# Kernel optimization log

Measured on AMD Instinct MI355X. Metric: run time of the kernel, lower is better.

The kernel has to match this reference:

```python
import jax, jax.numpy as jnp
import numpy as np

EPS = 0.1           # entropic regularization epsilon
MAX_ITER = 100
THRESH = 0.1        # early-stop threshold on mean |u - u_prev|
LOG_EPS = 1e-8


def setup_inputs() -> dict:
    key = jax.random.key(0)
    kx, ky = jax.random.split(key)
    x = jax.random.normal(kx, (8, 1024, 3), dtype=jnp.float32)
    y = jax.random.normal(ky, (8, 1024, 3), dtype=jnp.float32)
    return {"x": x, "y": y}


def _sqdist(x, y):
    # squared euclidean cost matrix [B, N, N]  (== torch.cdist(x,y,p=2)**2)
    x2 = jnp.sum(x * x, axis=-1)[:, :, None]
    y2 = jnp.sum(y * y, axis=-1)[:, None, :]
    xy = jnp.einsum("bnd,bmd->bnm", x, y)
    return jnp.maximum(x2 + y2 - 2.0 * xy, 0.0)


def reference(x, y):
    B, N, D = x.shape
    C = _sqdist(x, y)                      # [B, N, N]
    log_mu = jnp.log(1.0 / N + LOG_EPS)    # scalar (uniform marginals)
    log_nu = log_mu

    u0 = jnp.zeros((B, N), dtype=x.dtype)
    v0 = jnp.zeros((B, N), dtype=x.dtype)

    def step(carry, _):
        u, v, done = carry
        # u-update uses old v
        M1 = (u[:, :, None] + v[:, None, :] - C) / EPS          # [B,N,N]
        u_new = EPS * (log_mu - jax.nn.logsumexp(M1, axis=-1)) + u
        # v-update uses new u
        M2 = (u_new[:, :, None] + v[:, None, :] - C) / EPS
        v_new = EPS * (log_nu - jax.nn.logsumexp(M2, axis=-2)) + v
        # freeze once converged (mimics torch early break)
        u_out = jnp.where(done, u, u_new)
        v_out = jnp.where(done, v, v_new)
        err = jnp.mean(jnp.abs(u_out - u))
        done_new = done | (err < THRESH)
        return (u_out, v_out, done_new), None

    (u, v, _), _ = jax.lax.scan(step, (u0, v0, jnp.array(False)), None, length=MAX_ITER)

    PI = jnp.exp((u[:, :, None] + v[:, None, :] - C) / EPS)     # transport plan
    emd = jnp.sum(PI * C, axis=(-2, -1))                        # [B]
    return jnp.mean(emd)                                        # reduction='mean'
```

## Files before the change

kernel.cpp:

```cpp
#include <hip/hip_runtime.h>

typedef unsigned int uint_t;

constexpr int B = 8;
constexpr int N = 1024;
constexpr int NBLOCKS = 256;
constexpr int NTHREADS = 1024;
constexpr int NWAVES = NTHREADS / 64;
constexpr int BPB = NBLOCKS / B;
constexpr int SEG = N / BPB;
constexpr int RPW = SEG / NWAVES;
constexpr int KPL = N / 64;
constexpr int MAX_ITER = 100;
constexpr float THRESH = 0.1f;
constexpr float K2 = 14.42695040888963f;
constexpr float A2K = 2.0f * K2;
constexpr float NEPSLN2 = -0.06931471805599453f;
constexpr float EPSLOGMU = -0.693146156565634f;
constexpr uint_t MAGIC = 0xC0FFEE01u;

constexpr int OFF_U      = 0;
constexpr int OFF_V      = OFF_U + B * N;
constexpr int OFF_ERRBLK = OFF_V + B * N;
constexpr int OFF_ERRBAT = OFF_ERRBLK + 256;
constexpr int OFF_EMDBLK = OFF_ERRBAT + 800;
constexpr int OFF_EMDBAT = OFF_EMDBLK + 256;
constexpr int OFF_ZERO   = OFF_EMDBAT + 8;
constexpr int OFF_BARFLG = OFF_ZERO;
constexpr int OFF_ERRFLG = OFF_BARFLG + 256;
constexpr int OFF_EMDFLG = OFF_ERRFLG + 8;
constexpr int OFF_ZEROEND= OFF_EMDFLG + 8;
constexpr int OFF_INIT   = OFF_ZEROEND;

__device__ __forceinline__ float gload(const float* p) {
  return __hip_atomic_load(p, __ATOMIC_RELAXED, __HIP_MEMORY_SCOPE_AGENT);
}
__device__ __forceinline__ void gstore(float* p, float v) {
  __hip_atomic_store(p, v, __ATOMIC_RELAXED, __HIP_MEMORY_SCOPE_AGENT);
}
__device__ __forceinline__ uint_t lflag(const uint_t* p) {
  return __hip_atomic_load(p, __ATOMIC_RELAXED, __HIP_MEMORY_SCOPE_AGENT);
}
__device__ __forceinline__ void sflag_rel(uint_t* p, uint_t v) {
  __hip_atomic_store(p, v, __ATOMIC_RELEASE, __HIP_MEMORY_SCOPE_AGENT);
}

__device__ __forceinline__ float wsum(float v) {
#pragma unroll
  for (int o = 32; o; o >>= 1) v += __shfl_xor(v, o);
  return v;
}
__device__ __forceinline__ float wmax(float v) {
#pragma unroll
  for (int o = 32; o; o >>= 1) v = fmaxf(v, __shfl_xor(v, o));
  return v;
}

__device__ __forceinline__ float block_sum(float v, float* sh) {
  v = wsum(v);
  const int wave = threadIdx.x >> 6;
  const int lane = threadIdx.x & 63;
  if (lane == 0) sh[wave] = v;
  __syncthreads();
  float tot = 0.f;
#pragma unroll
  for (int w = 0; w < NWAVES; ++w) tot += sh[w];
  __syncthreads();
  return tot;
}

__device__ __forceinline__ void batch_barrier(uint_t* flg, int seg, uint_t epoch,
                                              int lane) {
  __syncthreads();
  if (threadIdx.x == 0) sflag_rel(&flg[seg], epoch);
  if (threadIdx.x < 64) {
    for (;;) {
      uint_t f = (lane < BPB) ? lflag(&flg[lane]) : epoch;
      if (__all(f >= epoch)) break;
      __builtin_amdgcn_s_sleep(1);
    }
  }
  __syncthreads();
}

template <bool TRACK>
__device__ __forceinline__ float half_compute(
    const float* __restrict__ cx, const float* __restrict__ cy,
    const float* __restrict__ cz, const float* __restrict__ cw,
    const float* __restrict__ rx, const float* __restrict__ ry,
    const float* __restrict__ rz, const float* __restrict__ rw,
    const float* __restrict__ pin, const float* __restrict__ pout_old,
    float (&pnew)[RPW], int i0, int lane, bool pin_zero, bool first_out) {
  float p2[KPL];
#pragma unroll
  for (int k = 0; k < KPL; ++k)
    p2[k] = pin_zero ? 0.f : gload(&pin[lane + (k << 6)]) * K2;

  float a0[RPW], a1[RPW], a2[RPW], X[RPW], m[RPW];
  float vals[RPW][KPL];
#pragma unroll
  for (int rr = 0; rr < RPW; ++rr) {
    a0[rr] = A2K * rx[i0 + rr]; a1[rr] = A2K * ry[i0 + rr];
    a2[rr] = A2K * rz[i0 + rr];
    X[rr] = -rw[i0 + rr];
    m[rr] = -3.4e38f;
  }
#pragma unroll
  for (int k = 0; k < KPL; ++k) {
    const int j = lane + (k << 6);
    float ccx = cx[j], ccy = cy[j], ccz = cz[j];
    float base = cw[j] + p2[k];
#pragma unroll
    for (int rr = 0; rr < RPW; ++rr) {
      float t = fmaf(a0[rr], ccx, fmaf(a1[rr], ccy, fmaf(a2[rr], ccz, base)));
      float val = fminf(t - X[rr], p2[k]);
      vals[rr][k] = val;
      m[rr] = fmaxf(m[rr], val);
    }
  }
  float err = 0.f;
#pragma unroll
  for (int rr = 0; rr < RPW; ++rr) {
    float mr = wmax(m[rr]);
    float s = 0.f;
#pragma unroll
    for (int k = 0; k < KPL; ++k)
      s += __builtin_amdgcn_exp2f(vals[rr][k] - mr);
    s = wsum(s);
    float pn = fmaf(NEPSLN2, mr + __builtin_amdgcn_logf(s), EPSLOGMU);
    pnew[rr] = pn;
    if (TRACK && lane == 0) {
      float old = first_out ? 0.f : gload(&pout_old[i0 + rr]);
      err += fabsf(pn - old);
    }
  }
  return err;
}

__device__ __forceinline__ void store_rows(float* p, const float (&pnew)[RPW],
                                           int i0, int lane) {
  if (lane == 0) {
#pragma unroll
    for (int rr = 0; rr < RPW; ++rr) gstore(&p[i0 + rr], pnew[rr]);
  }
}

__global__ void __launch_bounds__(NTHREADS, 4) sinkhorn_kernel(
    const float* __restrict__ xg, const float* __restrict__ yg,
    float* __restrict__ out, float* __restrict__ ws) {
  __shared__ float s_xx[N], s_xy[N], s_xz[N], s_xw[N];
  __shared__ float s_yx[N], s_yy[N], s_yz[N], s_yw[N];
  __shared__ float sh_red[NWAVES];

  const int bid = blockIdx.x;
  const int tid = threadIdx.x;
  const int b = bid & 7;
  const int seg = bid >> 3;
  const int wave = tid >> 6;
  const int lane = tid & 63;
  const int i0 = seg * SEG + wave * RPW;

  float* u = ws + OFF_U + b * N;
  float* v = ws + OFF_V + b * N;
  float* err_blk = ws + OFF_ERRBLK + b * 32;
  float* err_bat = ws + OFF_ERRBAT;
  float* emd_blk = ws + OFF_EMDBLK + b * 32;
  float* emd_bat = ws + OFF_EMDBAT;
  uint_t* bar_flg = (uint_t*)(ws + OFF_BARFLG) + b * 32;
  uint_t* err_flg = (uint_t*)(ws + OFF_ERRFLG);
  uint_t* emd_flg = (uint_t*)(ws + OFF_EMDFLG);
  uint_t* init_flag = (uint_t*)(ws + OFF_INIT);

  if (bid == 0) {
    uint_t* zb = (uint_t*)(ws + OFF_ZERO);
    for (int i = tid; i < OFF_ZEROEND - OFF_ZERO; i += NTHREADS)
      __hip_atomic_store(&zb[i], 0u, __ATOMIC_RELAXED, __HIP_MEMORY_SCOPE_AGENT);
    __syncthreads();
    if (tid == 0) sflag_rel(init_flag, MAGIC);
  }

  for (int p = tid; p < N; p += NTHREADS) {
    const float* xp = xg + (size_t)(b * N + p) * 3;
    float x0 = xp[0], x1 = xp[1], x2 = xp[2];
    s_xx[p] = x0; s_xy[p] = x1; s_xz[p] = x2;
    s_xw[p] = -K2 * (x0 * x0 + x1 * x1 + x2 * x2);
    const float* yp = yg + (size_t)(b * N + p) * 3;
    float y0 = yp[0], y1 = yp[1], y2 = yp[2];
    s_yx[p] = y0; s_yy[p] = y1; s_yz[p] = y2;
    s_yw[p] = -K2 * (y0 * y0 + y1 * y1 + y2 * y2);
  }
  __syncthreads();

  float un[RPW];
  float my_err = half_compute<true>(s_yx, s_yy, s_yz, s_yw,
                                    s_xx, s_xy, s_xz, s_xw,
                                    v, u, un, i0, lane,
                                    true, true);
  store_rows(u, un, i0, lane);
  float blk_err = block_sum(my_err, sh_red);
  if (tid == 0) gstore(&err_blk[seg], blk_err);

  if (tid == 0 && bid != 0)
    while (lflag(init_flag) != MAGIC) __builtin_amdgcn_s_sleep(2);
  __syncthreads();

  uint_t epoch = 0;
  int it = 0;
  for (;;) {
    ++epoch;
    batch_barrier(bar_flg, seg, epoch, lane);

    float vn[RPW];
    half_compute<false>(s_xx, s_xy, s_xz, s_xw,
                        s_yx, s_yy, s_yz, s_yw,
                        u, nullptr, vn, i0, lane, false, false);
    store_rows(v, vn, i0, lane);

    if (seg == 0 && tid < 64) {
      float e = (lane < BPB) ? gload(&err_blk[lane]) : 0.f;
      e = wsum(e);
      if (lane == 0) {
        gstore(&err_bat[it * B + b], e);
        sflag_rel(&err_flg[b], (uint_t)(it + 1));
      }
    }
    ++epoch;
    batch_barrier(bar_flg, seg, epoch, lane);

    if (it == MAX_ITER - 1) break;

    my_err = half_compute<true>(s_yx, s_yy, s_yz, s_yw,
                                s_xx, s_xy, s_xz, s_xw,
                                v, u, un, i0, lane, false, false);

    if (tid < 64) {
      const uint_t want = (uint_t)(it + 1);
      for (;;) {
        uint_t f = (lane < B) ? lflag(&err_flg[lane]) : want;
        if (__all(f >= want)) break;
        __builtin_amdgcn_s_sleep(1);
      }
      float e = (lane < B) ? gload(&err_bat[it * B + lane]) : 0.f;
      e = wsum(e);
      if (lane == 0) sh_red[0] = e;
    }
    __syncthreads();
    float tot = sh_red[0];
    __syncthreads();
    if (tot * (1.f / (B * N)) < THRESH) break;

    store_rows(u, un, i0, lane);
    blk_err = block_sum(my_err, sh_red);
    if (tid == 0) gstore(&err_blk[seg], blk_err);
    ++it;
  }

  float p2e[KPL];
#pragma unroll
  for (int k = 0; k < KPL; ++k) p2e[k] = gload(&v[lane + (k << 6)]) * K2;
  float acc = 0.f;
#pragma unroll
  for (int rr = 0; rr < RPW; ++rr) {
    const int i = i0 + rr;
    float a0 = A2K * s_xx[i], a1 = A2K * s_xy[i], a2 = A2K * s_xz[i];
    float X = -s_xw[i];
    float u2 = gload(&u[i]) * K2;
#pragma unroll
    for (int k = 0; k < KPL; ++k) {
      const int j = lane + (k << 6);
      float t = fmaf(a0, s_yx[j], fmaf(a1, s_yy[j], fmaf(a2, s_yz[j], s_yw[j])));
      float kc = fmaxf(X - t, 0.f);
      acc = fmaf(__builtin_amdgcn_exp2f(u2 + p2e[k] - kc), kc, acc);
    }
  }
  float blk = block_sum(acc, sh_red);
  const uint_t ef = epoch + 1;
  if (tid == 0) { gstore(&emd_blk[seg], blk); sflag_rel(&bar_flg[seg], ef); }

  if (seg == 0 && tid < 64) {
    for (;;) {
      uint_t f = (lane < BPB) ? lflag(&bar_flg[lane]) : ef;
      if (__all(f >= ef)) break;
      __builtin_amdgcn_s_sleep(1);
    }
    float e = (lane < BPB) ? gload(&emd_blk[lane]) : 0.f;
    e = wsum(e);
    if (lane == 0) { gstore(&emd_bat[b], e); sflag_rel(&emd_flg[b], 1u); }
  }
  if (bid == 0 && tid < 64) {
    for (;;) {
      uint_t f = (lane < B) ? lflag(&emd_flg[lane]) : 1u;
      if (__all(f >= 1u)) break;
      __builtin_amdgcn_s_sleep(1);
    }
    float e = (lane < B) ? gload(&emd_bat[lane]) : 0.f;
    e = wsum(e);
    if (lane == 0) out[0] = e * (1.f / (B * K2));
  }
}

extern "C" void kernel_launch(void* const* d_in, const int* in_sizes, int n_in,
                              void* d_out, int out_size, void* d_ws, size_t ws_size,
                              hipStream_t stream) {
  const float* x = (const float*)d_in[0];
  const float* y = (const float*)d_in[1];
  float* out = (float*)d_out;
  float* ws = (float*)d_ws;
  void* args[] = { (void*)&x, (void*)&y, (void*)&out, (void*)&ws };
  hipLaunchCooperativeKernel((const void*)sinkhorn_kernel,
                             dim3(NBLOCKS), dim3(NTHREADS), args, 0, stream);
}
```

Measured before the change: 134.3 us.

## Pack point data into float4 LDS arrays and halve block threads

Stores each point's coordinates and scaled norm as a single float4 in shared memory, so the inner loops issue one vector LDS read per column instead of four scalar reads. It also halves threads per block, which doubles the rows each wave handles and increases reuse of each loaded column across rows. The cost is higher register pressure from the larger vals array and fewer waves to hide latency, and the occupancy hint is lowered to match.

```diff
diff --git a/kernel.cpp b/kernel.cpp
--- a/kernel.cpp
+++ b/kernel.cpp
@@ -5,7 +5,7 @@
 constexpr int B = 8;
 constexpr int N = 1024;
 constexpr int NBLOCKS = 256;
-constexpr int NTHREADS = 1024;
+constexpr int NTHREADS = 512;
 constexpr int NWAVES = NTHREADS / 64;
 constexpr int BPB = NBLOCKS / B;
 constexpr int SEG = N / BPB;
@@ -85,10 +85,7 @@
 
 template <bool TRACK>
 __device__ __forceinline__ float half_compute(
-    const float* __restrict__ cx, const float* __restrict__ cy,
-    const float* __restrict__ cz, const float* __restrict__ cw,
-    const float* __restrict__ rx, const float* __restrict__ ry,
-    const float* __restrict__ rz, const float* __restrict__ rw,
+    const float4* __restrict__ c, const float4* __restrict__ r,
     const float* __restrict__ pin, const float* __restrict__ pout_old,
     float (&pnew)[RPW], int i0, int lane, bool pin_zero, bool first_out) {
   float p2[KPL];
@@ -100,19 +97,18 @@
   float vals[RPW][KPL];
 #pragma unroll
   for (int rr = 0; rr < RPW; ++rr) {
-    a0[rr] = A2K * rx[i0 + rr]; a1[rr] = A2K * ry[i0 + rr];
-    a2[rr] = A2K * rz[i0 + rr];
-    X[rr] = -rw[i0 + rr];
+    float4 r4 = r[i0 + rr];
+    a0[rr] = A2K * r4.x; a1[rr] = A2K * r4.y; a2[rr] = A2K * r4.z;
+    X[rr] = -r4.w;
     m[rr] = -3.4e38f;
   }
 #pragma unroll
   for (int k = 0; k < KPL; ++k) {
-    const int j = lane + (k << 6);
-    float ccx = cx[j], ccy = cy[j], ccz = cz[j];
-    float base = cw[j] + p2[k];
+    float4 c4 = c[lane + (k << 6)];
+    float base = c4.w + p2[k];
 #pragma unroll
     for (int rr = 0; rr < RPW; ++rr) {
-      float t = fmaf(a0[rr], ccx, fmaf(a1[rr], ccy, fmaf(a2[rr], ccz, base)));
+      float t = fmaf(a0[rr], c4.x, fmaf(a1[rr], c4.y, fmaf(a2[rr], c4.z, base)));
       float val = fminf(t - X[rr], p2[k]);
       vals[rr][k] = val;
       m[rr] = fmaxf(m[rr], val);
@@ -145,11 +141,11 @@
   }
 }
 
-__global__ void __launch_bounds__(NTHREADS, 4) sinkhorn_kernel(
+__global__ void __launch_bounds__(NTHREADS, 2) sinkhorn_kernel(
     const float* __restrict__ xg, const float* __restrict__ yg,
     float* __restrict__ out, float* __restrict__ ws) {
-  __shared__ float s_xx[N], s_xy[N], s_xz[N], s_xw[N];
-  __shared__ float s_yx[N], s_yy[N], s_yz[N], s_yw[N];
+  __shared__ float4 s_x4[N];
+  __shared__ float4 s_y4[N];
   __shared__ float sh_red[NWAVES];
 
   const int bid = blockIdx.x;
@@ -182,19 +178,15 @@
   for (int p = tid; p < N; p += NTHREADS) {
     const float* xp = xg + (size_t)(b * N + p) * 3;
     float x0 = xp[0], x1 = xp[1], x2 = xp[2];
-    s_xx[p] = x0; s_xy[p] = x1; s_xz[p] = x2;
-    s_xw[p] = -K2 * (x0 * x0 + x1 * x1 + x2 * x2);
+    s_x4[p] = make_float4(x0, x1, x2, -K2 * (x0 * x0 + x1 * x1 + x2 * x2));
     const float* yp = yg + (size_t)(b * N + p) * 3;
     float y0 = yp[0], y1 = yp[1], y2 = yp[2];
-    s_yx[p] = y0; s_yy[p] = y1; s_yz[p] = y2;
-    s_yw[p] = -K2 * (y0 * y0 + y1 * y1 + y2 * y2);
+    s_y4[p] = make_float4(y0, y1, y2, -K2 * (y0 * y0 + y1 * y1 + y2 * y2));
   }
   __syncthreads();
 
   float un[RPW];
-  float my_err = half_compute<true>(s_yx, s_yy, s_yz, s_yw,
-                                    s_xx, s_xy, s_xz, s_xw,
-                                    v, u, un, i0, lane,
+  float my_err = half_compute<true>(s_y4, s_x4, v, u, un, i0, lane,
                                     true, true);
   store_rows(u, un, i0, lane);
   float blk_err = block_sum(my_err, sh_red);
@@ -211,9 +203,7 @@
     batch_barrier(bar_flg, seg, epoch, lane);
 
     float vn[RPW];
-    half_compute<false>(s_xx, s_xy, s_xz, s_xw,
-                        s_yx, s_yy, s_yz, s_yw,
-                        u, nullptr, vn, i0, lane, false, false);
+    half_compute<false>(s_x4, s_y4, u, nullptr, vn, i0, lane, false, false);
     store_rows(v, vn, i0, lane);
 
     if (seg == 0 && tid < 64) {
@@ -229,9 +219,7 @@
 
     if (it == MAX_ITER - 1) break;
 
-    my_err = half_compute<true>(s_yx, s_yy, s_yz, s_yw,
-                                s_xx, s_xy, s_xz, s_xw,
-                                v, u, un, i0, lane, false, false);
+    my_err = half_compute<true>(s_y4, s_x4, v, u, un, i0, lane, false, false);
 
     if (tid < 64) {
       const uint_t want = (uint_t)(it + 1);
@@ -262,13 +250,14 @@
 #pragma unroll
   for (int rr = 0; rr < RPW; ++rr) {
     const int i = i0 + rr;
-    float a0 = A2K * s_xx[i], a1 = A2K * s_xy[i], a2 = A2K * s_xz[i];
-    float X = -s_xw[i];
+    float4 r4 = s_x4[i];
+    float a0 = A2K * r4.x, a1 = A2K * r4.y, a2 = A2K * r4.z;
+    float X = -r4.w;
     float u2 = gload(&u[i]) * K2;
 #pragma unroll
     for (int k = 0; k < KPL; ++k) {
-      const int j = lane + (k << 6);
-      float t = fmaf(a0, s_yx[j], fmaf(a1, s_yy[j], fmaf(a2, s_yz[j], s_yw[j])));
+      float4 c4 = s_y4[lane + (k << 6)];
+      float t = fmaf(a0, c4.x, fmaf(a1, c4.y, fmaf(a2, c4.z, c4.w)));
       float kc = fmaxf(X - t, 0.f);
       acc = fmaf(__builtin_amdgcn_exp2f(u2 + p2e[k] - kc), kc, acc);
     }
```

Result: faster. 124.5 us (-7.3%).

## Pack flag and payload into 64-bit words, halve block size, restructure barriers

Applied to the files above, without the earlier changes.

Replaces separate flag and data slots with 64-bit words that carry an epoch tag and a float payload. This removes the extra global load after each spin-wait and lets the per-block error ride on the barrier flag. Release-ordered stores become relaxed stores preceded by an explicit waitcnt drain, and the error ring is shortened to four slots. Block size drops from 1024 to 512 threads with launch bounds adjusted, which doubles rows per wave and register pressure. Correctness now depends on the drains ordering relaxed stores, which may be fragile across the memory hierarchy.

```diff
diff --git a/kernel.cpp b/kernel.cpp
--- a/kernel.cpp
+++ b/kernel.cpp
@@ -1,11 +1,12 @@
 #include <hip/hip_runtime.h>
 
 typedef unsigned int uint_t;
+typedef unsigned long long u64_t;
 
 constexpr int B = 8;
 constexpr int N = 1024;
 constexpr int NBLOCKS = 256;
-constexpr int NTHREADS = 1024;
+constexpr int NTHREADS = 512;
 constexpr int NWAVES = NTHREADS / 64;
 constexpr int BPB = NBLOCKS / B;
 constexpr int SEG = N / BPB;
@@ -19,18 +20,15 @@
 constexpr float EPSLOGMU = -0.693146156565634f;
 constexpr uint_t MAGIC = 0xC0FFEE01u;
 
-constexpr int OFF_U      = 0;
-constexpr int OFF_V      = OFF_U + B * N;
-constexpr int OFF_ERRBLK = OFF_V + B * N;
-constexpr int OFF_ERRBAT = OFF_ERRBLK + 256;
-constexpr int OFF_EMDBLK = OFF_ERRBAT + 800;
-constexpr int OFF_EMDBAT = OFF_EMDBLK + 256;
-constexpr int OFF_ZERO   = OFF_EMDBAT + 8;
-constexpr int OFF_BARFLG = OFF_ZERO;
-constexpr int OFF_ERRFLG = OFF_BARFLG + 256;
-constexpr int OFF_EMDFLG = OFF_ERRFLG + 8;
-constexpr int OFF_ZEROEND= OFF_EMDFLG + 8;
-constexpr int OFF_INIT   = OFF_ZEROEND;
+constexpr int OFF_U    = 0;
+constexpr int OFF_V    = OFF_U + B * N;
+constexpr int OFF_ZERO = OFF_V + B * N;
+constexpr int OFF_FLGA = OFF_ZERO;
+constexpr int OFF_FLGB = OFF_FLGA + 512;
+constexpr int OFF_ERRB = OFF_FLGB + 512;
+constexpr int OFF_EMD  = OFF_ERRB + 64;
+constexpr int OFF_ZEROEND = OFF_EMD + 16;
+constexpr int OFF_INIT = OFF_ZEROEND;
 
 __device__ __forceinline__ float gload(const float* p) {
   return __hip_atomic_load(p, __ATOMIC_RELAXED, __HIP_MEMORY_SCOPE_AGENT);
@@ -38,11 +36,22 @@
 __device__ __forceinline__ void gstore(float* p, float v) {
   __hip_atomic_store(p, v, __ATOMIC_RELAXED, __HIP_MEMORY_SCOPE_AGENT);
 }
-__device__ __forceinline__ uint_t lflag(const uint_t* p) {
+__device__ __forceinline__ uint_t l32(const uint_t* p) {
   return __hip_atomic_load(p, __ATOMIC_RELAXED, __HIP_MEMORY_SCOPE_AGENT);
 }
-__device__ __forceinline__ void sflag_rel(uint_t* p, uint_t v) {
-  __hip_atomic_store(p, v, __ATOMIC_RELEASE, __HIP_MEMORY_SCOPE_AGENT);
+__device__ __forceinline__ void s32(uint_t* p, uint_t v) {
+  __hip_atomic_store(p, v, __ATOMIC_RELAXED, __HIP_MEMORY_SCOPE_AGENT);
+}
+__device__ __forceinline__ u64_t l64(const u64_t* p) {
+  return __hip_atomic_load(p, __ATOMIC_RELAXED, __HIP_MEMORY_SCOPE_AGENT);
+}
+__device__ __forceinline__ void s64(u64_t* p, u64_t v) {
+  __hip_atomic_store(p, v, __ATOMIC_RELAXED, __HIP_MEMORY_SCOPE_AGENT);
+}
+__device__ __forceinline__ void drain() { __builtin_amdgcn_s_waitcnt(0); }
+
+__device__ __forceinline__ u64_t pk64(uint_t tag, float v) {
+  return ((u64_t)tag << 32) | (u64_t)__float_as_uint(v);
 }
 
 __device__ __forceinline__ float wsum(float v) {
@@ -67,20 +76,6 @@
   for (int w = 0; w < NWAVES; ++w) tot += sh[w];
   __syncthreads();
   return tot;
-}
-
-__device__ __forceinline__ void batch_barrier(uint_t* flg, int seg, uint_t epoch,
-                                              int lane) {
-  __syncthreads();
-  if (threadIdx.x == 0) sflag_rel(&flg[seg], epoch);
-  if (threadIdx.x < 64) {
-    for (;;) {
-      uint_t f = (lane < BPB) ? lflag(&flg[lane]) : epoch;
-      if (__all(f >= epoch)) break;
-      __builtin_amdgcn_s_sleep(1);
-    }
-  }
-  __syncthreads();
 }
 
 template <bool TRACK>
@@ -145,7 +140,7 @@
   }
 }
 
-__global__ void __launch_bounds__(NTHREADS, 4) sinkhorn_kernel(
+__global__ void __launch_bounds__(NTHREADS, 2) sinkhorn_kernel(
     const float* __restrict__ xg, const float* __restrict__ yg,
     float* __restrict__ out, float* __restrict__ ws) {
   __shared__ float s_xx[N], s_xy[N], s_xz[N], s_xw[N];
@@ -162,21 +157,19 @@
 
   float* u = ws + OFF_U + b * N;
   float* v = ws + OFF_V + b * N;
-  float* err_blk = ws + OFF_ERRBLK + b * 32;
-  float* err_bat = ws + OFF_ERRBAT;
-  float* emd_blk = ws + OFF_EMDBLK + b * 32;
-  float* emd_bat = ws + OFF_EMDBAT;
-  uint_t* bar_flg = (uint_t*)(ws + OFF_BARFLG) + b * 32;
-  uint_t* err_flg = (uint_t*)(ws + OFF_ERRFLG);
-  uint_t* emd_flg = (uint_t*)(ws + OFF_EMDFLG);
+  u64_t* flgA = (u64_t*)(ws + OFF_FLGA) + b * 32;
+  u64_t* flgB = (u64_t*)(ws + OFF_FLGB) + b * 32;
+  u64_t* errB = (u64_t*)(ws + OFF_ERRB);
+  u64_t* emdB = (u64_t*)(ws + OFF_EMD);
   uint_t* init_flag = (uint_t*)(ws + OFF_INIT);
 
   if (bid == 0) {
-    uint_t* zb = (uint_t*)(ws + OFF_ZERO);
-    for (int i = tid; i < OFF_ZEROEND - OFF_ZERO; i += NTHREADS)
-      __hip_atomic_store(&zb[i], 0u, __ATOMIC_RELAXED, __HIP_MEMORY_SCOPE_AGENT);
-    __syncthreads();
-    if (tid == 0) sflag_rel(init_flag, MAGIC);
+    u64_t* zb = (u64_t*)(ws + OFF_ZERO);
+    for (int i = tid; i < (OFF_ZEROEND - OFF_ZERO) / 2; i += NTHREADS)
+      s64(&zb[i], 0ull);
+    drain();
+    __syncthreads();
+    if (tid == 0) s32(init_flag, MAGIC);
   }
 
   for (int p = tid; p < N; p += NTHREADS) {
@@ -197,35 +190,48 @@
                                     v, u, un, i0, lane,
                                     true, true);
   store_rows(u, un, i0, lane);
+  drain();
   float blk_err = block_sum(my_err, sh_red);
-  if (tid == 0) gstore(&err_blk[seg], blk_err);
-
   if (tid == 0 && bid != 0)
-    while (lflag(init_flag) != MAGIC) __builtin_amdgcn_s_sleep(2);
+    while (l32(init_flag) != MAGIC) __builtin_amdgcn_s_sleep(2);
   __syncthreads();
-
-  uint_t epoch = 0;
+  if (tid == 0) s64(&flgA[seg], pk64(1u, blk_err));
+
   int it = 0;
   for (;;) {
-    ++epoch;
-    batch_barrier(bar_flg, seg, epoch, lane);
+    const uint_t want = (uint_t)(it + 1);
+
+    if (wave == 0) {
+      float pay;
+      for (;;) {
+        u64_t pk = (lane < BPB) ? l64(&flgA[lane]) : ~0ull;
+        if (__all((uint_t)(pk >> 32) >= want)) { pay = __uint_as_float((uint_t)pk); break; }
+        __builtin_amdgcn_s_sleep(1);
+      }
+      if (seg == 0) {
+        float e = wsum((lane < BPB) ? pay : 0.f);
+        if (lane == 0) s64(&errB[(it & 3) * 8 + b], pk64(want, e));
+      }
+    }
+    __syncthreads();
 
     float vn[RPW];
     half_compute<false>(s_xx, s_xy, s_xz, s_xw,
                         s_yx, s_yy, s_yz, s_yw,
                         u, nullptr, vn, i0, lane, false, false);
     store_rows(v, vn, i0, lane);
-
-    if (seg == 0 && tid < 64) {
-      float e = (lane < BPB) ? gload(&err_blk[lane]) : 0.f;
-      e = wsum(e);
-      if (lane == 0) {
-        gstore(&err_bat[it * B + b], e);
-        sflag_rel(&err_flg[b], (uint_t)(it + 1));
+    drain();
+    __syncthreads();
+    if (tid == 0) s64(&flgB[seg], pk64(want, 0.f));
+
+    if (wave == 0) {
+      for (;;) {
+        u64_t pk = (lane < BPB) ? l64(&flgB[lane]) : ~0ull;
+        if (__all((uint_t)(pk >> 32) >= want)) break;
+        __builtin_amdgcn_s_sleep(1);
       }
     }
-    ++epoch;
-    batch_barrier(bar_flg, seg, epoch, lane);
+    __syncthreads();
 
     if (it == MAX_ITER - 1) break;
 
@@ -233,15 +239,14 @@
                                 s_xx, s_xy, s_xz, s_xw,
                                 v, u, un, i0, lane, false, false);
 
-    if (tid < 64) {
-      const uint_t want = (uint_t)(it + 1);
+    if (wave == 0) {
+      float pay;
       for (;;) {
-        uint_t f = (lane < B) ? lflag(&err_flg[lane]) : want;
-        if (__all(f >= want)) break;
+        u64_t pk = (lane < B) ? l64(&errB[(it & 3) * 8 + lane]) : ~0ull;
+        if (__all((uint_t)(pk >> 32) >= want)) { pay = __uint_as_float((uint_t)pk); break; }
         __builtin_amdgcn_s_sleep(1);
       }
-      float e = (lane < B) ? gload(&err_bat[it * B + lane]) : 0.f;
-      e = wsum(e);
+      float e = wsum((lane < B) ? pay : 0.f);
       if (lane == 0) sh_red[0] = e;
     }
     __syncthreads();
@@ -250,8 +255,9 @@
     if (tot * (1.f / (B * N)) < THRESH) break;
 
     store_rows(u, un, i0, lane);
+    drain();
     blk_err = block_sum(my_err, sh_red);
-    if (tid == 0) gstore(&err_blk[seg], blk_err);
+    if (tid == 0) s64(&flgA[seg], pk64((uint_t)(it + 2), blk_err));
     ++it;
   }
 
@@ -274,27 +280,27 @@
     }
   }
   float blk = block_sum(acc, sh_red);
-  const uint_t ef = epoch + 1;
-  if (tid == 0) { gstore(&emd_blk[seg], blk); sflag_rel(&bar_flg[seg], ef); }
-
-  if (seg == 0 && tid < 64) {
+  const uint_t ef = (uint_t)(it + 2);
+  if (tid == 0) s64(&flgB[seg], pk64(ef, blk));
+
+  if (seg == 0 && wave == 0) {
+    float pay;
     for (;;) {
-      uint_t f = (lane < BPB) ? lflag(&bar_flg[lane]) : ef;
-      if (__all(f >= ef)) break;
+      u64_t pk = (lane < BPB) ? l64(&flgB[lane]) : ~0ull;
+      if (__all((uint_t)(pk >> 32) >= ef)) { pay = __uint_as_float((uint_t)pk); break; }
       __builtin_amdgcn_s_sleep(1);
     }
-    float e = (lane < BPB) ? gload(&emd_blk[lane]) : 0.f;
-    e = wsum(e);
-    if (lane == 0) { gstore(&emd_bat[b], e); sflag_rel(&emd_flg[b], 1u); }
-  }
-  if (bid == 0 && tid < 64) {
+    float e = wsum((lane < BPB) ? pay : 0.f);
+    if (lane == 0) s64(&emdB[b], pk64(1u, e));
+  }
+  if (bid == 0 && wave == 0) {
+    float pay;
     for (;;) {
-      uint_t f = (lane < B) ? lflag(&emd_flg[lane]) : 1u;
-      if (__all(f >= 1u)) break;
+      u64_t pk = (lane < B) ? l64(&emdB[lane]) : ~0ull;
+      if (__all((uint_t)(pk >> 32) >= 1u)) { pay = __uint_as_float((uint_t)pk); break; }
       __builtin_amdgcn_s_sleep(1);
     }
-    float e = (lane < B) ? gload(&emd_bat[lane]) : 0.f;
-    e = wsum(e);
+    float e = wsum((lane < B) ? pay : 0.f);
     if (lane == 0) out[0] = e * (1.f / (B * K2));
   }
 }
```

Measured after the change: 110.3 us. 1.22x faster.
